# Optimization experiments

Hardware: AMD Instinct MI355X
Metric: run time of the kernel (lower is better)

## Reference

```python
import jax, jax.numpy as jnp
import numpy as np

D_MODEL = 1024
NUM_HEADS = 16
ENERGY_SCALE = 0.1
LN_EPS = 1e-5


def layernorm(x, gamma, beta):
    mu = jnp.mean(x, axis=-1, keepdims=True)
    var = jnp.var(x, axis=-1, keepdims=True)
    return (x - mu) * jax.lax.rsqrt(var + LN_EPS) * gamma + beta


def setup_inputs() -> dict:
    key = jax.random.key(0)
    ks = jax.random.split(key, 8)
    B, L, D = 2, 2048, D_MODEL
    s = 0.02
    return {
        "x": jax.random.normal(ks[0], (B, L, D), dtype=jnp.float32),
        "wq": jax.random.normal(ks[1], (D, D), dtype=jnp.float32) * s,
        "wk": jax.random.normal(ks[2], (D, D), dtype=jnp.float32) * s,
        "wv": jax.random.normal(ks[3], (D, D), dtype=jnp.float32) * s,
        "wo_w": jax.random.normal(ks[4], (D, D), dtype=jnp.float32) * s,
        "wo_b": jnp.zeros((D,), dtype=jnp.float32),
        "ep_w": jax.random.normal(ks[5], (D, D), dtype=jnp.float32) * s,
        "ep_b": jnp.zeros((D,), dtype=jnp.float32),
        "en_g": jnp.ones((D,), dtype=jnp.float32),
        "en_b": jnp.zeros((D,), dtype=jnp.float32),
        "ln_g": jnp.ones((D,), dtype=jnp.float32),
        "ln_b": jnp.zeros((D,), dtype=jnp.float32),
    }


def reference(x, wq, wk, wv, wo_w, wo_b, ep_w, ep_b, en_g, en_b, ln_g, ln_b):
    B, L, D = x.shape
    H, dk = NUM_HEADS, D // NUM_HEADS
    # Linear projections (torch convention: y = x @ W^T), split heads -> [B,H,L,dk]
    q = (x @ wq.T).reshape(B, L, H, dk).transpose(0, 2, 1, 3)
    k = (x @ wk.T).reshape(B, L, H, dk).transpose(0, 2, 1, 3)
    v = (x @ wv.T).reshape(B, L, H, dk).transpose(0, 2, 1, 3)
    scores = jnp.einsum("bhld,bhmd->bhlm", q, k) / jnp.sqrt(jnp.float32(dk))
    # Energy bias: ef @ ef^T as a proper GEMM (same math as the broadcast-mul-sum)
    ef = layernorm(x @ ep_w.T + ep_b, en_g, en_b)
    energy_bias = jnp.einsum("bld,bmd->blm", ef, ef)  # [B,L,L]
    scores = scores + ENERGY_SCALE * energy_bias[:, None, :, :]
    attn = jax.nn.softmax(scores, axis=-1)  # dropout is identity in eval mode
    ctx = jnp.einsum("bhlm,bhmd->bhld", attn, v)
    ctx = ctx.transpose(0, 2, 1, 3).reshape(B, L, D)
    out = ctx @ wo_w.T + wo_b
    return layernorm(out + x, ln_g, ln_b), attn
```

## Files before the change

### kernel.cpp

```cpp
#include <hip/hip_runtime.h>
#include <math.h>

#define D_MODEL 1024
#define NUM_HEADS 16
#define DK 64
#define L_SEQ 2048
#define BATCH 2
#define LN_EPS 1e-5f
#define ENERGY_SCALE 0.1f

typedef __attribute__((ext_vector_type(8))) short short8;
typedef __attribute__((ext_vector_type(4))) float f32x4;
typedef __attribute__((address_space(1))) const unsigned int gas_u32;
typedef __attribute__((address_space(3))) unsigned int las_u32;

__device__ __forceinline__ float waveReduceSum(float v) {
#pragma unroll
    for (int off = 32; off > 0; off >>= 1) v += __shfl_xor(v, off, 64);
    return v;
}

__device__ __forceinline__ unsigned short f2bf(float f) {
    unsigned int u = __float_as_uint(f);
    u += 0x7fff + ((u >> 16) & 1);
    return (unsigned short)(u >> 16);
}
__device__ __forceinline__ float bf2f(unsigned short u) {
    return __uint_as_float((unsigned int)u << 16);
}

__global__ __launch_bounds__(256) void cvt6(
    const float* s0, const float* s1, const float* s2,
    const float* s3, const float* s4, const float* s5,
    unsigned short* d0, unsigned short* d1, unsigned short* d2,
    unsigned short* d3, unsigned short* d4, unsigned short* d5,
    long long n0, long long n1, long long n2, long long n3, long long n4, long long n5)
{
    const float* s; unsigned short* d; long long n;
    switch (blockIdx.y) {
        case 0: s = s0; d = d0; n = n0; break;
        case 1: s = s1; d = d1; n = n1; break;
        case 2: s = s2; d = d2; n = n2; break;
        case 3: s = s3; d = d3; n = n3; break;
        case 4: s = s4; d = d4; n = n4; break;
        default: s = s5; d = d5; n = n5; break;
    }
    long long i = ((long long)blockIdx.x * 256 + threadIdx.x) * 4;
    if (i >= n) return;
    float4 v = *(const float4*)(s + i);
    ushort4 o;
    o.x = f2bf(v.x); o.y = f2bf(v.y); o.z = f2bf(v.z); o.w = f2bf(v.w);
    *(ushort4*)(d + i) = o;
}

__global__ __launch_bounds__(256) void gemm_bf16(
    const unsigned short* __restrict__ A, const unsigned short* __restrict__ B,
    const float* __restrict__ bias, float* __restrict__ Cf, unsigned short* __restrict__ Ch,
    int N, int K, long long sA, long long sB, long long sC)
{
    A += (long long)blockIdx.z * sA;
    B += (long long)blockIdx.z * sB;
    __shared__ unsigned short As[128 * 64];
    __shared__ unsigned short Bs[128 * 64];
    const int tid = threadIdx.x;
    const int lane = tid & 63, w = tid >> 6;
    const int quad = lane >> 4, col = lane & 15;
    const int wm = w & 1, wn = w >> 1;
    const int row0 = blockIdx.y * 128, col0 = blockIdx.x * 128;

    const int lr = lane >> 3, lc = lane & 7;
    const int gcs = (lc ^ lr) * 8;

    f32x4 acc[4][4];
#pragma unroll
    for (int mt = 0; mt < 4; mt++)
#pragma unroll
        for (int nt = 0; nt < 4; nt++) acc[mt][nt] = (f32x4){0.f, 0.f, 0.f, 0.f};

    for (int k0 = 0; k0 < K; k0 += 64) {
        __syncthreads();
#pragma unroll
        for (int p = 0; p < 4; p++) {
            const int rb = w * 32 + p * 8;
            __builtin_amdgcn_global_load_lds(
                (gas_u32*)(A + (long long)(row0 + rb + lr) * K + k0 + gcs),
                (las_u32*)(As + rb * 64), 16, 0, 0);
            __builtin_amdgcn_global_load_lds(
                (gas_u32*)(B + (long long)(col0 + rb + lr) * K + k0 + gcs),
                (las_u32*)(Bs + rb * 64), 16, 0, 0);
        }
        __syncthreads();
#pragma unroll
        for (int kc = 0; kc < 2; kc++) {
            const int csw = ((quad + 4 * kc) ^ (col & 7)) * 8;
            short8 af[4], bfr[4];
#pragma unroll
            for (int mt = 0; mt < 4; mt++)
                af[mt] = *(const short8*)(As + (wm * 64 + mt * 16 + col) * 64 + csw);
#pragma unroll
            for (int nt = 0; nt < 4; nt++)
                bfr[nt] = *(const short8*)(Bs + (wn * 64 + nt * 16 + col) * 64 + csw);
#pragma unroll
            for (int mt = 0; mt < 4; mt++)
#pragma unroll
                for (int nt = 0; nt < 4; nt++)
                    acc[mt][nt] = __builtin_amdgcn_mfma_f32_16x16x32_bf16(af[mt], bfr[nt], acc[mt][nt], 0, 0, 0);
        }
    }

#pragma unroll
    for (int mt = 0; mt < 4; mt++)
#pragma unroll
        for (int nt = 0; nt < 4; nt++)
#pragma unroll
            for (int reg = 0; reg < 4; reg++) {
                long long row = row0 + wm * 64 + mt * 16 + quad * 4 + reg;
                int c = col0 + wn * 64 + nt * 16 + col;
                float v = acc[mt][nt][reg];
                if (bias) v += bias[c];
                if (Cf) Cf[blockIdx.z * sC + row * N + c] = v;
                else    Ch[blockIdx.z * sC + row * N + c] = f2bf(v);
            }
}

__global__ __launch_bounds__(256) void proj_gemm(
    const unsigned short* __restrict__ Xh,
    const unsigned short* __restrict__ wqh, const unsigned short* __restrict__ wkh,
    const unsigned short* __restrict__ wvh, const unsigned short* __restrict__ eph,
    const float* __restrict__ ep_b,
    unsigned short* __restrict__ Qh, unsigned short* __restrict__ Kh,
    unsigned short* __restrict__ Vf, float* __restrict__ EP)
{
    const unsigned short* B;
    switch (blockIdx.z) {
        case 0: B = wqh; break;
        case 1: B = wkh; break;
        case 2: B = wvh; break;
        default: B = eph; break;
    }
    __shared__ unsigned short As[128 * 64];
    __shared__ unsigned short Bs[128 * 64];
    const int tid = threadIdx.x;
    const int lane = tid & 63, w = tid >> 6;
    const int quad = lane >> 4, col = lane & 15;
    const int wm = w & 1, wn = w >> 1;
    const int row0 = blockIdx.y * 128, col0 = blockIdx.x * 128;
    const int K = D_MODEL, N = D_MODEL;

    const int lr = lane >> 3, lc = lane & 7;
    const int gcs = (lc ^ lr) * 8;

    f32x4 acc[4][4];
#pragma unroll
    for (int mt = 0; mt < 4; mt++)
#pragma unroll
        for (int nt = 0; nt < 4; nt++) acc[mt][nt] = (f32x4){0.f, 0.f, 0.f, 0.f};

    for (int k0 = 0; k0 < K; k0 += 64) {
        __syncthreads();
#pragma unroll
        for (int p = 0; p < 4; p++) {
            const int rb = w * 32 + p * 8;
            __builtin_amdgcn_global_load_lds(
                (gas_u32*)(Xh + (long long)(row0 + rb + lr) * K + k0 + gcs),
                (las_u32*)(As + rb * 64), 16, 0, 0);
            __builtin_amdgcn_global_load_lds(
                (gas_u32*)(B + (long long)(col0 + rb + lr) * K + k0 + gcs),
                (las_u32*)(Bs + rb * 64), 16, 0, 0);
        }
        __syncthreads();
#pragma unroll
        for (int kc = 0; kc < 2; kc++) {
            const int csw = ((quad + 4 * kc) ^ (col & 7)) * 8;
            short8 af[4], bfr[4];
#pragma unroll
            for (int mt = 0; mt < 4; mt++)
                af[mt] = *(const short8*)(As + (wm * 64 + mt * 16 + col) * 64 + csw);
#pragma unroll
            for (int nt = 0; nt < 4; nt++)
                bfr[nt] = *(const short8*)(Bs + (wn * 64 + nt * 16 + col) * 64 + csw);
#pragma unroll
            for (int mt = 0; mt < 4; mt++)
#pragma unroll
                for (int nt = 0; nt < 4; nt++)
                    acc[mt][nt] = __builtin_amdgcn_mfma_f32_16x16x32_bf16(af[mt], bfr[nt], acc[mt][nt], 0, 0, 0);
        }
    }

    unsigned short* Hout = (blockIdx.z == 0) ? Qh : (blockIdx.z == 1) ? Kh : Vf;
#pragma unroll
    for (int mt = 0; mt < 4; mt++)
#pragma unroll
        for (int nt = 0; nt < 4; nt++)
#pragma unroll
            for (int reg = 0; reg < 4; reg++) {
                long long row = row0 + wm * 64 + mt * 16 + quad * 4 + reg;
                int c = col0 + wn * 64 + nt * 16 + col;
                float v = acc[mt][nt][reg];
                if (blockIdx.z == 3) EP[row * N + c] = v + ep_b[c];
                else                 Hout[row * N + c] = f2bf(v);
            }
}

__global__ __launch_bounds__(256) void ln_rows(
    const float* __restrict__ in, const float* __restrict__ res,
    const float* __restrict__ g, const float* __restrict__ bta,
    float* __restrict__ outf, unsigned short* __restrict__ outh)
{
    const long long row = blockIdx.x;
    const float* ip = in + row * D_MODEL;
    const float* rp = res ? res + row * D_MODEL : nullptr;
    const int tid = threadIdx.x;
    float vals[4];
    float s = 0.f, ss = 0.f;
#pragma unroll
    for (int j = 0; j < 4; j++) {
        int idx = tid + j * 256;
        float v = ip[idx];
        if (rp) v += rp[idx];
        vals[j] = v; s += v; ss += v * v;
    }
    __shared__ float sred[4], ssred[4];
    s = waveReduceSum(s); ss = waveReduceSum(ss);
    int wave = tid >> 6, lane = tid & 63;
    if (lane == 0) { sred[wave] = s; ssred[wave] = ss; }
    __syncthreads();
    float ts = sred[0] + sred[1] + sred[2] + sred[3];
    float tss = ssred[0] + ssred[1] + ssred[2] + ssred[3];
    float mu = ts * (1.f / D_MODEL);
    float var = tss * (1.f / D_MODEL) - mu * mu;
    float rs = rsqrtf(var + LN_EPS);
#pragma unroll
    for (int j = 0; j < 4; j++) {
        int idx = tid + j * 256;
        float o = (vals[j] - mu) * rs * g[idx] + bta[idx];
        if (outf) outf[row * D_MODEL + idx] = o;
        else      outh[row * D_MODEL + idx] = f2bf(o);
    }
}

__global__ __launch_bounds__(256) void transpose_v(
    const unsigned short* __restrict__ V, unsigned short* __restrict__ Vt)
{
    const int m0 = blockIdx.x * 64, h = blockIdx.y, b = blockIdx.z;
    __shared__ unsigned int t[64][65];
    const int tid = threadIdx.x;
    {
        int r = tid >> 4, c4 = (tid & 15) * 4;
#pragma unroll
        for (int i = 0; i < 4; i++) {
            int row = r + i * 16;
            ushort4 v = *(const ushort4*)(V + ((long long)b * L_SEQ + m0 + row) * D_MODEL + h * DK + c4);
            t[row][c4] = v.x; t[row][c4 + 1] = v.y; t[row][c4 + 2] = v.z; t[row][c4 + 3] = v.w;
        }
    }
    __syncthreads();
    const int lane = tid & 63, wv = tid >> 6;
#pragma unroll
    for (int i = 0; i < 16; i++) {
        int d = wv * 16 + i;
        Vt[(((long long)(b * NUM_HEADS + h)) * DK + d) * L_SEQ + m0 + lane] = (unsigned short)t[lane][d];
    }
}

__global__ __launch_bounds__(256) void eb_stats(
    const unsigned short* __restrict__ EBh, float* __restrict__ ebmax, float* __restrict__ ebtmax)
{
    const long long row = blockIdx.x;
    const unsigned short* p = EBh + row * L_SEQ;
    const int tid = threadIdx.x;
    short8 v = *(const short8*)(p + tid * 8);
    float m = bf2f((unsigned short)v[0]);
#pragma unroll
    for (int j = 1; j < 8; j++) m = fmaxf(m, bf2f((unsigned short)v[j]));
    m = fmaxf(m, __shfl_xor(m, 1, 64));
    m = fmaxf(m, __shfl_xor(m, 2, 64));
    m = fmaxf(m, __shfl_xor(m, 4, 64));
    if ((tid & 7) == 0) ebtmax[row * 32 + (tid >> 3)] = m;
    m = fmaxf(m, __shfl_xor(m, 8, 64));
    m = fmaxf(m, __shfl_xor(m, 16, 64));
    m = fmaxf(m, __shfl_xor(m, 32, 64));
    __shared__ float red[4];
    if ((tid & 63) == 0) red[tid >> 6] = m;
    __syncthreads();
    if (tid == 0)
        ebmax[row] = fmaxf(fmaxf(red[0], red[1]), fmaxf(red[2], red[3]));
}

__global__ __launch_bounds__(256) void qk_stats(
    const unsigned short* __restrict__ Qh, const unsigned short* __restrict__ Kh,
    float* __restrict__ qn, float* __restrict__ kn)
{
    const int l0 = blockIdx.x * 64, h = blockIdx.y, b = blockIdx.z;
    const int tid = threadIdx.x;
    const int r = tid >> 2, p4 = (tid & 3) * 16;
    const unsigned short* q = Qh + ((long long)b * L_SEQ + l0 + r) * D_MODEL + h * DK + p4;
    const unsigned short* k = Kh + ((long long)b * L_SEQ + l0 + r) * D_MODEL + h * DK + p4;
    float sq = 0.f, sk = 0.f;
#pragma unroll
    for (int i = 0; i < 16; i++) {
        float qv = bf2f(q[i]); sq += qv * qv;
        float kv = bf2f(k[i]); sk += kv * kv;
    }
    sq += __shfl_xor(sq, 1, 64); sq += __shfl_xor(sq, 2, 64);
    sk += __shfl_xor(sk, 1, 64); sk += __shfl_xor(sk, 2, 64);
    if ((tid & 3) == 0) {
        long long idx = ((long long)(b * NUM_HEADS + h)) * L_SEQ + l0 + r;
        qn[idx] = sqrtf(sq);
        kn[idx] = sqrtf(sk);
    }
}

__global__ __launch_bounds__(256) void kstats2(
    const float* __restrict__ kn, float* __restrict__ kmax, float* __restrict__ ktmax)
{
    const long long bh = blockIdx.x;
    const float* p = kn + bh * L_SEQ;
    const int tid = threadIdx.x;
    float4 a = *(const float4*)(p + tid * 8);
    float4 c = *(const float4*)(p + tid * 8 + 4);
    float m = fmaxf(fmaxf(fmaxf(a.x, a.y), fmaxf(a.z, a.w)),
                    fmaxf(fmaxf(c.x, c.y), fmaxf(c.z, c.w)));
    m = fmaxf(m, __shfl_xor(m, 1, 64));
    m = fmaxf(m, __shfl_xor(m, 2, 64));
    m = fmaxf(m, __shfl_xor(m, 4, 64));
    if ((tid & 7) == 0) ktmax[bh * 32 + (tid >> 3)] = m;
    m = fmaxf(m, __shfl_xor(m, 8, 64));
    m = fmaxf(m, __shfl_xor(m, 16, 64));
    m = fmaxf(m, __shfl_xor(m, 32, 64));
    __shared__ float red[4];
    if ((tid & 63) == 0) red[tid >> 6] = m;
    __syncthreads();
    if (tid == 0)
        kmax[bh] = fmaxf(fmaxf(red[0], red[1]), fmaxf(red[2], red[3]));
}

__global__ __launch_bounds__(64) void skip_mask(
    const float* __restrict__ ebmax, const float* __restrict__ ebtmax,
    const float* __restrict__ qn, const float* __restrict__ kmax,
    const float* __restrict__ ktmax, unsigned int* __restrict__ skipm)
{
    const int l0 = blockIdx.x * 64, h = blockIdx.y, b = blockIdx.z;
    const int tid = threadIdx.x;
    const int row = l0 + tid;
    const int bh = b * NUM_HEADS + h;
    float q = qn[(long long)bh * L_SEQ + row];
    float Mh = ENERGY_SCALE * ebmax[(long long)b * L_SEQ + row] + q * kmax[bh] * 0.125f + 0.02f;
    const float* ebt = ebtmax + ((long long)b * L_SEQ + row) * 32;
    const float* ktm = ktmax + bh * 32;
    unsigned int m = 0;
    for (int t = 0; t < 32; t++) {
        float ub = ENERGY_SCALE * ebt[t] + q * ktm[t] * 0.125f;
        unsigned long long bal = __ballot(ub < Mh - 45.0f);
        if (bal == ~0ull) m |= (1u << t);
    }
    if (tid == 0) skipm[bh * 32 + blockIdx.x] = m;
}

__global__ __launch_bounds__(256) void attn_mfma(
    const unsigned short* __restrict__ Qh, const unsigned short* __restrict__ Kh,
    const unsigned short* __restrict__ Vt, const unsigned short* __restrict__ EBh,
    const float* __restrict__ ebmax, const float* __restrict__ qn,
    const float* __restrict__ kmax, const unsigned int* __restrict__ skipm,
    float* __restrict__ attn_out, unsigned short* __restrict__ CTXh)
{
    __shared__ unsigned short Ks[2][64 * 64];
    __shared__ unsigned short Vts[64 * 64];
    __shared__ unsigned short Ps[4 * 16 * 72];

    const int tid = threadIdx.x;
    const int lane = tid & 63, w = tid >> 6;
    const int quad = lane >> 4, col = lane & 15;
    const int l0 = blockIdx.x * 64;
    const int h = blockIdx.y, b = blockIdx.z;

    const unsigned int sm = skipm[(b * NUM_HEADS + h) * 32 + blockIdx.x];

    const unsigned short* kbase = Kh + ((long long)b * L_SEQ) * D_MODEL + h * DK;
    const unsigned short* vbase = Vt + ((long long)(b * NUM_HEADS + h)) * DK * L_SEQ;

    const int lr = lane >> 3, lc = lane & 7;
    const int gsw = (lc ^ lr) * 8;

    auto nxt = [&](int t) -> int {
        unsigned int rem = ~sm;
        if (t >= 0) rem &= (t >= 31) ? 0u : (0xFFFFFFFFu << (t + 1));
        return rem ? (int)__builtin_ctz(rem) : -1;
    };
    const int t0 = nxt(-1);

    if (t0 >= 0) {
#pragma unroll
        for (int p = 0; p < 2; p++) {
            const int rb = w * 8 + p * 32;
            __builtin_amdgcn_global_load_lds(
                (gas_u32*)(kbase + (long long)(t0 * 64 + rb + lr) * D_MODEL + gsw),
                (las_u32*)(&Ks[0][rb * 64]), 16, 0, 0);
        }
    }

    {
        float* zbase = attn_out + (((long long)(b * NUM_HEADS + h)) * L_SEQ + l0) * L_SEQ;
        const int zc = (tid & 15) * 4;
        const int zr = tid >> 4;
        const float4 zv = {0.f, 0.f, 0.f, 0.f};
        for (int t = 0; t < 32; t++) {
            if (!(sm & (1u << t))) continue;
            float* tb = zbase + t * 64 + zc;
#pragma unroll
            for (int rr = 0; rr < 4; rr++)
                *(float4*)(tb + (long long)(rr * 16 + zr) * L_SEQ) = zv;
        }
    }

    short8 aq[2];
    {
        const unsigned short* qrow = Qh + ((long long)b * L_SEQ + l0 + w * 16 + col) * D_MODEL + h * DK;
        aq[0] = *(const short8*)(qrow + quad * 8);
        aq[1] = *(const short8*)(qrow + 32 + quad * 8);
    }

    float Mhat[4];
    {
        const float km = kmax[b * NUM_HEADS + h];
#pragma unroll
        for (int reg = 0; reg < 4; reg++) {
            int row = l0 + w * 16 + quad * 4 + reg;
            float qb = qn[((long long)(b * NUM_HEADS + h)) * L_SEQ + row];
            Mhat[reg] = ENERGY_SCALE * ebmax[(long long)b * L_SEQ + row] +
                        qb * km * 0.125f + 0.02f;
        }
    }

    const unsigned short* ebp = EBh + ((long long)b * L_SEQ + l0 + w * 16 + quad * 4) * L_SEQ + col;

    __syncthreads();

    float rowSacc[4] = {0.f, 0.f, 0.f, 0.f};
    int cur = 0;
    for (int t = t0; t >= 0; ) {
        const int tn = nxt(t);
        if (tn >= 0) {
#pragma unroll
            for (int p = 0; p < 2; p++) {
                const int rb = w * 8 + p * 32;
                __builtin_amdgcn_global_load_lds(
                    (gas_u32*)(kbase + (long long)(tn * 64 + rb + lr) * D_MODEL + gsw),
                    (las_u32*)(&Ks[cur ^ 1][rb * 64]), 16, 0, 0);
            }
        }
        const int m0 = t * 64;

        f32x4 acc[4];
#pragma unroll
        for (int nt = 0; nt < 4; nt++) acc[nt] = (f32x4){0.f, 0.f, 0.f, 0.f};
        __builtin_amdgcn_s_setprio(1);
#pragma unroll
        for (int nt = 0; nt < 4; nt++)
#pragma unroll
            for (int kc = 0; kc < 2; kc++) {
                short8 bk = *(const short8*)(&Ks[cur][((nt * 16 + col) << 6) +
                                                     (((quad + 4 * kc) ^ (col & 7)) << 3)]);
                acc[nt] = __builtin_amdgcn_mfma_f32_16x16x32_bf16(aq[kc], bk, acc[nt], 0, 0, 0);
            }
        __builtin_amdgcn_s_setprio(0);
#pragma unroll
        for (int nt = 0; nt < 4; nt++)
#pragma unroll
            for (int reg = 0; reg < 4; reg++) {
                float e = bf2f(ebp[(long long)reg * L_SEQ + m0 + nt * 16]);
                float s = acc[nt][reg] * 0.125f + ENERGY_SCALE * e;
                rowSacc[reg] += __expf(s - Mhat[reg]);
            }
        __syncthreads();
        cur ^= 1;
        t = tn;
    }

    float invS[4];
#pragma unroll
    for (int reg = 0; reg < 4; reg++) {
        float v = rowSacc[reg];
#pragma unroll
        for (int off = 8; off > 0; off >>= 1) v += __shfl_xor(v, off, 64);
        invS[reg] = 1.f / v;
    }

    cur = 0;
    if (t0 >= 0) {
#pragma unroll
        for (int p = 0; p < 2; p++) {
            const int rb = w * 8 + p * 32;
            __builtin_amdgcn_global_load_lds(
                (gas_u32*)(kbase + (long long)(t0 * 64 + rb + lr) * D_MODEL + gsw),
                (las_u32*)(&Ks[0][rb * 64]), 16, 0, 0);
        }
    }
    __syncthreads();

    f32x4 ctx[4];
#pragma unroll
    for (int nt = 0; nt < 4; nt++) ctx[nt] = (f32x4){0.f, 0.f, 0.f, 0.f};

    unsigned short* Psw = Ps + w * 16 * 72;
    float* aob = attn_out + (((long long)(b * NUM_HEADS + h)) * L_SEQ + l0 + w * 16 + quad * 4) * L_SEQ + col;

    for (int t = t0; t >= 0; ) {
        const int tn = nxt(t);
        const int m0 = t * 64;

#pragma unroll
        for (int p = 0; p < 2; p++) {
            const int rb = w * 8 + p * 32;
            __builtin_amdgcn_global_load_lds(
                (gas_u32*)(vbase + (long long)(rb + lr) * L_SEQ + m0 + gsw),
                (las_u32*)(&Vts[rb * 64]), 16, 0, 0);
        }
        if (tn >= 0) {
#pragma unroll
            for (int p = 0; p < 2; p++) {
                const int rb = w * 8 + p * 32;
                __builtin_amdgcn_global_load_lds(
                    (gas_u32*)(kbase + (long long)(tn * 64 + rb + lr) * D_MODEL + gsw),
                    (las_u32*)(&Ks[cur ^ 1][rb * 64]), 16, 0, 0);
            }
        }

        f32x4 acc[4];
#pragma unroll
        for (int nt = 0; nt < 4; nt++) acc[nt] = (f32x4){0.f, 0.f, 0.f, 0.f};
        __builtin_amdgcn_s_setprio(1);
#pragma unroll
        for (int nt = 0; nt < 4; nt++)
#pragma unroll
            for (int kc = 0; kc < 2; kc++) {
                short8 bk = *(const short8*)(&Ks[cur][((nt * 16 + col) << 6) +
                                                     (((quad + 4 * kc) ^ (col & 7)) << 3)]);
                acc[nt] = __builtin_amdgcn_mfma_f32_16x16x32_bf16(aq[kc], bk, acc[nt], 0, 0, 0);
            }
        __builtin_amdgcn_s_setprio(0);

#pragma unroll
        for (int nt = 0; nt < 4; nt++)
#pragma unroll
            for (int reg = 0; reg < 4; reg++) {
                float e = bf2f(ebp[(long long)reg * L_SEQ + m0 + nt * 16]);
                float s = acc[nt][reg] * 0.125f + ENERGY_SCALE * e;
                float p = __expf(s - Mhat[reg]) * invS[reg];
                acc[nt][reg] = p;
                Psw[(quad * 4 + reg) * 72 + nt * 16 + col] = f2bf(p);
            }
        __syncthreads();

#pragma unroll
        for (int nt = 0; nt < 4; nt++)
#pragma unroll
            for (int reg = 0; reg < 4; reg++)
                aob[(long long)reg * L_SEQ + m0 + nt * 16] = acc[nt][reg];

        short8 ap[2];
#pragma unroll
        for (int kc = 0; kc < 2; kc++)
            ap[kc] = *(const short8*)(Psw + col * 72 + quad * 8 + kc * 32);
        __builtin_amdgcn_s_setprio(1);
#pragma unroll
        for (int nt = 0; nt < 4; nt++)
#pragma unroll
            for (int kc = 0; kc < 2; kc++) {
                short8 bv = *(const short8*)(&Vts[((nt * 16 + col) << 6) +
                                                  (((quad + 4 * kc) ^ (col & 7)) << 3)]);
                ctx[nt] = __builtin_amdgcn_mfma_f32_16x16x32_bf16(ap[kc], bv, ctx[nt], 0, 0, 0);
            }
        __builtin_amdgcn_s_setprio(0);
        __syncthreads();
        cur ^= 1;
        t = tn;
    }

#pragma unroll
    for (int nt = 0; nt < 4; nt++)
#pragma unroll
        for (int reg = 0; reg < 4; reg++)
            CTXh[((long long)b * L_SEQ + l0 + w * 16 + quad * 4 + reg) * D_MODEL + h * DK + nt * 16 + col] =
                f2bf(ctx[nt][reg]);
}

extern "C" void kernel_launch(void* const* d_in, const int* in_sizes, int n_in,
                              void* d_out, int out_size, void* d_ws, size_t ws_size,
                              hipStream_t stream) {
    const float* x    = (const float*)d_in[0];
    const float* wq   = (const float*)d_in[1];
    const float* wk   = (const float*)d_in[2];
    const float* wv   = (const float*)d_in[3];
    const float* wo_w = (const float*)d_in[4];
    const float* wo_b = (const float*)d_in[5];
    const float* ep_w = (const float*)d_in[6];
    const float* ep_b = (const float*)d_in[7];
    const float* en_g = (const float*)d_in[8];
    const float* en_b = (const float*)d_in[9];
    const float* ln_g = (const float*)d_in[10];
    const float* ln_b = (const float*)d_in[11];

    float* out_final = (float*)d_out;
    float* attn_out  = out_final + (long long)BATCH * L_SEQ * D_MODEL;

    const long long MD = (long long)BATCH * L_SEQ * D_MODEL;
    const long long WN = (long long)D_MODEL * D_MODEL;
    const long long BH = (long long)BATCH * NUM_HEADS;
    const long long LL = (long long)BATCH * L_SEQ * L_SEQ;

    unsigned short* EBh = (unsigned short*)d_ws;
    float* EP = (float*)(EBh + LL);
    unsigned short* Xh   = (unsigned short*)(EP + MD);
    unsigned short* Qh   = Xh + MD;
    unsigned short* Kh   = Qh + MD;
    unsigned short* Vf   = Kh + MD;
    unsigned short* Vt   = Vf + MD;
    unsigned short* EFh  = Vt + MD;
    unsigned short* CTXh = EFh + MD;
    unsigned short* wqh  = CTXh + MD;
    unsigned short* wkh  = wqh + WN;
    unsigned short* wvh  = wkh + WN;
    unsigned short* eph  = wvh + WN;
    unsigned short* woh  = eph + WN;
    float* ebmax  = (float*)(woh + WN);
    float* qn     = ebmax + (long long)BATCH * L_SEQ;
    float* kn     = qn + BH * L_SEQ;
    float* kmax   = kn + BH * L_SEQ;
    float* ktmax  = kmax + BH;
    float* ebtmax = ktmax + BH * 32;
    unsigned int* skipm = (unsigned int*)(ebtmax + (long long)BATCH * L_SEQ * 32);
    float* OUT = EP;

    const int M = BATCH * L_SEQ;
    dim3 blk(256);

    cvt6<<<dim3((unsigned)(MD / 1024), 6), blk, 0, stream>>>(
        x, wq, wk, wv, ep_w, wo_w, Xh, wqh, wkh, wvh, eph, woh,
        MD, WN, WN, WN, WN, WN);

    proj_gemm<<<dim3(D_MODEL / 128, M / 128, 4), blk, 0, stream>>>(
        Xh, wqh, wkh, wvh, eph, ep_b, Qh, Kh, Vf, EP);

    ln_rows<<<dim3(M), blk, 0, stream>>>(EP, nullptr, en_g, en_b, nullptr, EFh);

    gemm_bf16<<<dim3(L_SEQ / 128, L_SEQ / 128, BATCH), blk, 0, stream>>>(
        EFh, EFh, nullptr, nullptr, EBh, L_SEQ, D_MODEL,
        (long long)L_SEQ * D_MODEL, (long long)L_SEQ * D_MODEL,
        (long long)L_SEQ * L_SEQ);

    qk_stats<<<dim3(L_SEQ / 64, NUM_HEADS, BATCH), blk, 0, stream>>>(Qh, Kh, qn, kn);
    kstats2<<<dim3((unsigned)BH), blk, 0, stream>>>(kn, kmax, ktmax);
    eb_stats<<<dim3(M), blk, 0, stream>>>(EBh, ebmax, ebtmax);
    skip_mask<<<dim3(L_SEQ / 64, NUM_HEADS, BATCH), dim3(64), 0, stream>>>(
        ebmax, ebtmax, qn, kmax, ktmax, skipm);

    transpose_v<<<dim3(L_SEQ / 64, NUM_HEADS, BATCH), blk, 0, stream>>>(Vf, Vt);

    attn_mfma<<<dim3(L_SEQ / 64, NUM_HEADS, BATCH), blk, 0, stream>>>(
        Qh, Kh, Vt, EBh, ebmax, qn, kmax, skipm, attn_out, CTXh);

    gemm_bf16<<<dim3(D_MODEL / 128, M / 128, 1), blk, 0, stream>>>(
        CTXh, woh, wo_b, OUT, nullptr, D_MODEL, D_MODEL, 0, 0, 0);

    ln_rows<<<dim3(M), blk, 0, stream>>>(OUT, x, ln_g, ln_b, out_final, nullptr);
}
```

Before: 749.2 us.

## Fuse Q/K norms and energy-bias tile maxima into GEMM epilogues; nontemporal stores

Q/K row-norm computation moves into the projection GEMM epilogue, and the per-64-column tile maxima of the energy bias move into the energy GEMM epilogue. This removes the separate qk_stats and eb_stats kernels and their re-reads of Q, K and the L×L bias matrix. The per-row max is now computed inside skip_mask from the tile maxima. The large attention-probability, zero-fill and final output writes use nontemporal stores to reduce cache pollution. The cost is extra shuffle reductions in the GEMM epilogues and a 32-float register array in skip_mask.

```diff
diff --git a/kernel.cpp b/kernel.cpp
--- a/kernel.cpp
+++ b/kernel.cpp
@@ -56,7 +56,8 @@
 __global__ __launch_bounds__(256) void gemm_bf16(
     const unsigned short* __restrict__ A, const unsigned short* __restrict__ B,
     const float* __restrict__ bias, float* __restrict__ Cf, unsigned short* __restrict__ Ch,
-    int N, int K, long long sA, long long sB, long long sC)
+    int N, int K, long long sA, long long sB, long long sC,
+    float* __restrict__ ebtmax)
 {
     A += (long long)blockIdx.z * sA;
     B += (long long)blockIdx.z * sB;
@@ -121,6 +122,32 @@
                 if (Cf) Cf[blockIdx.z * sC + row * N + c] = v;
                 else    Ch[blockIdx.z * sC + row * N + c] = f2bf(v);
             }
+
+    if (ebtmax) {
+        const int tcol = blockIdx.x * 2 + wn;
+#pragma unroll
+        for (int mt = 0; mt < 4; mt++) {
+            float mx[4];
+#pragma unroll
+            for (int reg = 0; reg < 4; reg++) mx[reg] = acc[mt][0][reg];
+#pragma unroll
+            for (int nt = 1; nt < 4; nt++)
+#pragma unroll
+                for (int reg = 0; reg < 4; reg++)
+                    mx[reg] = fmaxf(mx[reg], acc[mt][nt][reg]);
+#pragma unroll
+            for (int off = 8; off > 0; off >>= 1)
+#pragma unroll
+                for (int reg = 0; reg < 4; reg++)
+                    mx[reg] = fmaxf(mx[reg], __shfl_xor(mx[reg], off, 64));
+            if (col == 0) {
+                long long rowg = (long long)blockIdx.z * L_SEQ + row0 + wm * 64 + mt * 16 + quad * 4;
+#pragma unroll
+                for (int reg = 0; reg < 4; reg++)
+                    ebtmax[(rowg + reg) * 32 + tcol] = bf2f(f2bf(mx[reg]));
+            }
+        }
+    }
 }
 
 __global__ __launch_bounds__(256) void proj_gemm(
@@ -129,7 +156,8 @@
     const unsigned short* __restrict__ wvh, const unsigned short* __restrict__ eph,
     const float* __restrict__ ep_b,
     unsigned short* __restrict__ Qh, unsigned short* __restrict__ Kh,
-    unsigned short* __restrict__ Vf, float* __restrict__ EP)
+    unsigned short* __restrict__ Vf, float* __restrict__ EP,
+    float* __restrict__ qn, float* __restrict__ kn)
 {
     const unsigned short* B;
     switch (blockIdx.z) {
@@ -200,6 +228,35 @@
                 if (blockIdx.z == 3) EP[row * N + c] = v + ep_b[c];
                 else                 Hout[row * N + c] = f2bf(v);
             }
+
+    if (blockIdx.z <= 1) {
+        float* dst = (blockIdx.z == 0) ? qn : kn;
+        const int hh = blockIdx.x * 2 + wn;
+#pragma unroll
+        for (int mt = 0; mt < 4; mt++) {
+            float s2[4];
+#pragma unroll
+            for (int reg = 0; reg < 4; reg++) s2[reg] = 0.f;
+#pragma unroll
+            for (int nt = 0; nt < 4; nt++)
+#pragma unroll
+                for (int reg = 0; reg < 4; reg++)
+                    s2[reg] += acc[mt][nt][reg] * acc[mt][nt][reg];
+#pragma unroll
+            for (int off = 8; off > 0; off >>= 1)
+#pragma unroll
+                for (int reg = 0; reg < 4; reg++)
+                    s2[reg] += __shfl_xor(s2[reg], off, 64);
+            if (col == 0) {
+                int row = row0 + wm * 64 + mt * 16 + quad * 4;
+                int bb = row >> 11, l = row & (L_SEQ - 1);
+                float4 o;
+                o.x = sqrtf(s2[0]); o.y = sqrtf(s2[1]);
+                o.z = sqrtf(s2[2]); o.w = sqrtf(s2[3]);
+                *(float4*)(dst + ((long long)(bb * NUM_HEADS + hh)) * L_SEQ + l) = o;
+            }
+        }
+    }
 }
 
 __global__ __launch_bounds__(256) void ln_rows(
@@ -234,7 +291,7 @@
     for (int j = 0; j < 4; j++) {
         int idx = tid + j * 256;
         float o = (vals[j] - mu) * rs * g[idx] + bta[idx];
-        if (outf) outf[row * D_MODEL + idx] = o;
+        if (outf) __builtin_nontemporal_store(o, outf + row * D_MODEL + idx);
         else      outh[row * D_MODEL + idx] = f2bf(o);
     }
 }
@@ -260,54 +317,6 @@
     for (int i = 0; i < 16; i++) {
         int d = wv * 16 + i;
         Vt[(((long long)(b * NUM_HEADS + h)) * DK + d) * L_SEQ + m0 + lane] = (unsigned short)t[lane][d];
-    }
-}
-
-__global__ __launch_bounds__(256) void eb_stats(
-    const unsigned short* __restrict__ EBh, float* __restrict__ ebmax, float* __restrict__ ebtmax)
-{
-    const long long row = blockIdx.x;
-    const unsigned short* p = EBh + row * L_SEQ;
-    const int tid = threadIdx.x;
-    short8 v = *(const short8*)(p + tid * 8);
-    float m = bf2f((unsigned short)v[0]);
-#pragma unroll
-    for (int j = 1; j < 8; j++) m = fmaxf(m, bf2f((unsigned short)v[j]));
-    m = fmaxf(m, __shfl_xor(m, 1, 64));
-    m = fmaxf(m, __shfl_xor(m, 2, 64));
-    m = fmaxf(m, __shfl_xor(m, 4, 64));
-    if ((tid & 7) == 0) ebtmax[row * 32 + (tid >> 3)] = m;
-    m = fmaxf(m, __shfl_xor(m, 8, 64));
-    m = fmaxf(m, __shfl_xor(m, 16, 64));
-    m = fmaxf(m, __shfl_xor(m, 32, 64));
-    __shared__ float red[4];
-    if ((tid & 63) == 0) red[tid >> 6] = m;
-    __syncthreads();
-    if (tid == 0)
-        ebmax[row] = fmaxf(fmaxf(red[0], red[1]), fmaxf(red[2], red[3]));
-}
-
-__global__ __launch_bounds__(256) void qk_stats(
-    const unsigned short* __restrict__ Qh, const unsigned short* __restrict__ Kh,
-    float* __restrict__ qn, float* __restrict__ kn)
-{
-    const int l0 = blockIdx.x * 64, h = blockIdx.y, b = blockIdx.z;
-    const int tid = threadIdx.x;
-    const int r = tid >> 2, p4 = (tid & 3) * 16;
-    const unsigned short* q = Qh + ((long long)b * L_SEQ + l0 + r) * D_MODEL + h * DK + p4;
-    const unsigned short* k = Kh + ((long long)b * L_SEQ + l0 + r) * D_MODEL + h * DK + p4;
-    float sq = 0.f, sk = 0.f;
-#pragma unroll
-    for (int i = 0; i < 16; i++) {
-        float qv = bf2f(q[i]); sq += qv * qv;
-        float kv = bf2f(k[i]); sk += kv * kv;
-    }
-    sq += __shfl_xor(sq, 1, 64); sq += __shfl_xor(sq, 2, 64);
-    sk += __shfl_xor(sk, 1, 64); sk += __shfl_xor(sk, 2, 64);
-    if ((tid & 3) == 0) {
-        long long idx = ((long long)(b * NUM_HEADS + h)) * L_SEQ + l0 + r;
-        qn[idx] = sqrtf(sq);
-        kn[idx] = sqrtf(sk);
     }
 }
 
@@ -336,21 +345,30 @@
 }
 
 __global__ __launch_bounds__(64) void skip_mask(
-    const float* __restrict__ ebmax, const float* __restrict__ ebtmax,
-    const float* __restrict__ qn, const float* __restrict__ kmax,
-    const float* __restrict__ ktmax, unsigned int* __restrict__ skipm)
+    const float* __restrict__ ebtmax, const float* __restrict__ qn,
+    const float* __restrict__ kmax, const float* __restrict__ ktmax,
+    unsigned int* __restrict__ skipm, float* __restrict__ ebmax)
 {
     const int l0 = blockIdx.x * 64, h = blockIdx.y, b = blockIdx.z;
     const int tid = threadIdx.x;
     const int row = l0 + tid;
     const int bh = b * NUM_HEADS + h;
+    const float* ebt = ebtmax + ((long long)b * L_SEQ + row) * 32;
+    float ebr[32];
+#pragma unroll
+    for (int t = 0; t < 32; t++) ebr[t] = ebt[t];
+    float mx = ebr[0];
+#pragma unroll
+    for (int t = 1; t < 32; t++) mx = fmaxf(mx, ebr[t]);
+    if (blockIdx.y == 0) ebmax[(long long)b * L_SEQ + row] = mx;
+
     float q = qn[(long long)bh * L_SEQ + row];
-    float Mh = ENERGY_SCALE * ebmax[(long long)b * L_SEQ + row] + q * kmax[bh] * 0.125f + 0.02f;
-    const float* ebt = ebtmax + ((long long)b * L_SEQ + row) * 32;
+    float Mh = ENERGY_SCALE * mx + q * kmax[bh] * 0.125f + 0.02f;
     const float* ktm = ktmax + bh * 32;
     unsigned int m = 0;
+#pragma unroll
     for (int t = 0; t < 32; t++) {
-        float ub = ENERGY_SCALE * ebt[t] + q * ktm[t] * 0.125f;
+        float ub = ENERGY_SCALE * ebr[t] + q * ktm[t] * 0.125f;
         unsigned long long bal = __ballot(ub < Mh - 45.0f);
         if (bal == ~0ull) m |= (1u << t);
     }
@@ -403,13 +421,13 @@
         float* zbase = attn_out + (((long long)(b * NUM_HEADS + h)) * L_SEQ + l0) * L_SEQ;
         const int zc = (tid & 15) * 4;
         const int zr = tid >> 4;
-        const float4 zv = {0.f, 0.f, 0.f, 0.f};
+        const f32x4 zv = {0.f, 0.f, 0.f, 0.f};
         for (int t = 0; t < 32; t++) {
             if (!(sm & (1u << t))) continue;
             float* tb = zbase + t * 64 + zc;
 #pragma unroll
             for (int rr = 0; rr < 4; rr++)
-                *(float4*)(tb + (long long)(rr * 16 + zr) * L_SEQ) = zv;
+                __builtin_nontemporal_store(zv, (f32x4*)(tb + (long long)(rr * 16 + zr) * L_SEQ));
         }
     }
 
@@ -556,7 +574,8 @@
         for (int nt = 0; nt < 4; nt++)
 #pragma unroll
             for (int reg = 0; reg < 4; reg++)
-                aob[(long long)reg * L_SEQ + m0 + nt * 16] = acc[nt][reg];
+                __builtin_nontemporal_store(acc[nt][reg],
+                    aob + (long long)reg * L_SEQ + m0 + nt * 16);
 
         short8 ap[2];
 #pragma unroll
@@ -640,20 +659,18 @@
         MD, WN, WN, WN, WN, WN);
 
     proj_gemm<<<dim3(D_MODEL / 128, M / 128, 4), blk, 0, stream>>>(
-        Xh, wqh, wkh, wvh, eph, ep_b, Qh, Kh, Vf, EP);
+        Xh, wqh, wkh, wvh, eph, ep_b, Qh, Kh, Vf, EP, qn, kn);
 
     ln_rows<<<dim3(M), blk, 0, stream>>>(EP, nullptr, en_g, en_b, nullptr, EFh);
 
     gemm_bf16<<<dim3(L_SEQ / 128, L_SEQ / 128, BATCH), blk, 0, stream>>>(
         EFh, EFh, nullptr, nullptr, EBh, L_SEQ, D_MODEL,
         (long long)L_SEQ * D_MODEL, (long long)L_SEQ * D_MODEL,
-        (long long)L_SEQ * L_SEQ);
-
-    qk_stats<<<dim3(L_SEQ / 64, NUM_HEADS, BATCH), blk, 0, stream>>>(Qh, Kh, qn, kn);
+        (long long)L_SEQ * L_SEQ, ebtmax);
+
     kstats2<<<dim3((unsigned)BH), blk, 0, stream>>>(kn, kmax, ktmax);
-    eb_stats<<<dim3(M), blk, 0, stream>>>(EBh, ebmax, ebtmax);
     skip_mask<<<dim3(L_SEQ / 64, NUM_HEADS, BATCH), dim3(64), 0, stream>>>(
-        ebmax, ebtmax, qn, kmax, ktmax, skipm);
+        ebtmax, qn, kmax, ktmax, skipm, ebmax);
 
     transpose_v<<<dim3(L_SEQ / 64, NUM_HEADS, BATCH), blk, 0, stream>>>(Vf, Vt);
 
@@ -661,7 +678,7 @@
         Qh, Kh, Vt, EBh, ebmax, qn, kmax, skipm, attn_out, CTXh);
 
     gemm_bf16<<<dim3(D_MODEL / 128, M / 128, 1), blk, 0, stream>>>(
-        CTXh, woh, wo_b, OUT, nullptr, D_MODEL, D_MODEL, 0, 0, 0);
+        CTXh, woh, wo_b, OUT, nullptr, D_MODEL, D_MODEL, 0, 0, 0, nullptr);
 
     ln_rows<<<dim3(M), blk, 0, stream>>>(OUT, x, ln_g, ln_b, out_final, nullptr);
 }
```

Result: no change. 743.0 us (-0.8%).
